# Performance work log

Hardware: AMD Instinct MI355X
Metric: run time of the kernel (lower is better)

## Reference

```python
import jax, jax.numpy as jnp
import numpy as np

N_NODES = 100000
N_EDGES = 1600000
IN_CH = 128
EMB = 64


def _init_linear(key, fan_in, fan_out):
    kw, kb = jax.random.split(key)
    scale = 1.0 / np.sqrt(fan_in)
    W = jax.random.uniform(kw, (fan_in, fan_out), jnp.float32, -scale, scale)
    b = jax.random.uniform(kb, (fan_out,), jnp.float32, -scale, scale)
    return W, b


def setup_inputs() -> dict:
    key = jax.random.key(0)
    ks = jax.random.split(key, 6)
    x = jax.random.normal(ks[0], (N_NODES, IN_CH), jnp.float32)
    edge_index = jax.random.randint(ks[1], (2, N_EDGES), 0, N_NODES)
    batch = jnp.zeros((N_NODES,), jnp.int32)
    # conv1 MLP: in_channels -> 32 -> 64 ; conv2 MLP: 64 -> 64 -> embedding_dim
    W1, b1 = _init_linear(ks[2], IN_CH, 32)
    W2, b2 = _init_linear(ks[3], 32, 64)
    W3, b3 = _init_linear(ks[4], 64, 64)
    W4, b4 = _init_linear(ks[5], 64, EMB)
    return {"x": x, "edge_index": edge_index, "batch": batch,
            "W1": W1, "b1": b1, "W2": W2, "b2": b2,
            "W3": W3, "b3": b3, "W4": W4, "b4": b4}


def _mlp(h, Wa, ba, Wb, bb):
    # PyG MLP: Linear -> act -> Linear (plain last layer)
    return jax.nn.relu(h @ Wa + ba) @ Wb + bb


def _gin_conv(x, src, dst, Wa, ba, Wb, bb):
    # out_i = MLP((1+eps)*x_i + sum_{j->i} x_j), eps = 0 (GINConv default)
    agg = jax.ops.segment_sum(x[src], dst, num_segments=N_NODES)  # [N, d]
    return _mlp(x + agg, Wa, ba, Wb, bb)


def reference(x, edge_index, batch, W1, b1, W2, b2, W3, b3, W4, b4):
    src, dst = edge_index[0], edge_index[1]
    h = jax.nn.relu(_gin_conv(x, src, dst, W1, b1, W2, b2))  # [N, 64]
    h = jax.nn.relu(_gin_conv(h, src, dst, W3, b3, W4, b4))  # [N, EMB]
    # batch is overwritten with zeros in the original forward -> single graph
    pooled = jnp.mean(h, axis=0, keepdims=True)  # [1, EMB]
    return h, pooled
```

## Files before the change

kernel.cpp:

```cpp
#include <hip/hip_runtime.h>

#define NN 100000
#define NE 1600000
#define NLB 256
#define CHUNK (NE / NLB)
#define NB 196
#define BN 512

__device__ __forceinline__ float bf2f(unsigned short u) {
    return __uint_as_float(((unsigned int)u) << 16);
}
__device__ __forceinline__ unsigned short f2bf(float f) {
    unsigned int u = __float_as_uint(f);
    return (unsigned short)((u + 0x7FFFu + ((u >> 16) & 1u)) >> 16);
}

__global__ __launch_bounds__(256) void k_front(const int* __restrict__ src,
                                               const int* __restrict__ dst,
                                               int* __restrict__ pairs,
                                               int* __restrict__ tstart,
                                               int* __restrict__ tcnt,
                                               int* __restrict__ btot,
                                               const float* __restrict__ x,
                                               const float* __restrict__ W1,
                                               unsigned short* __restrict__ z1) {
    __shared__ float Ws[128 * 32];
    __shared__ float xs[32][129];
    __shared__ int cnt[NB];
    __shared__ int sc[256];
    __shared__ int cur[NB];
    int tid = threadIdx.x;
    if (blockIdx.x < NLB) {
        int blk = blockIdx.x;
        int e0 = blk * CHUNK;
        for (int i = tid; i < NB; i += 256) cnt[i] = 0;
        __syncthreads();
        for (int i = tid; i < CHUNK; i += 256) atomicAdd(&cnt[dst[e0 + i] >> 9], 1);
        __syncthreads();
        sc[tid] = (tid < NB) ? cnt[tid] : 0;
        __syncthreads();
        for (int off = 1; off < 256; off <<= 1) {
            int v = (tid >= off) ? sc[tid - off] : 0;
            __syncthreads();
            sc[tid] += v;
            __syncthreads();
        }
        if (tid < NB) {
            int excl = sc[tid] - cnt[tid];
            cur[tid] = excl;
            tstart[blk * NB + tid] = excl;
            tcnt[blk * NB + tid]   = cnt[tid];
            atomicAdd(&btot[tid], cnt[tid]);
        }
        __syncthreads();
        for (int i = tid; i < CHUNK; i += 256) {
            int d = dst[e0 + i], s = src[e0 + i];
            int p = atomicAdd(&cur[d >> 9], 1);
            pairs[e0 + p] = ((d & (BN - 1)) << 17) | s;
        }
    } else {
        int bid = blockIdx.x - NLB;
        for (int i = tid; i < 1024; i += 256) {
            float4 w = ((const float4*)W1)[i];
            float* d = &Ws[i * 4];
            d[0] = w.x; d[1] = w.y; d[2] = w.z; d[3] = w.w;
        }
        int n_loc = tid >> 3;
        int j0    = (tid & 7) * 4;
        for (int base = bid * 32; base < NN; base += 1024 * 32) {
            __syncthreads();
            for (int t = tid; t < 1024; t += 256) {
                int n = t >> 5, c = t & 31;
                float4 v = ((const float4*)(x + (size_t)(base + n) * 128))[c];
                float* d = &xs[n][c * 4];
                d[0] = v.x; d[1] = v.y; d[2] = v.z; d[3] = v.w;
            }
            __syncthreads();
            float a0 = 0.f, a1 = 0.f, a2 = 0.f, a3 = 0.f;
            #pragma unroll 8
            for (int k = 0; k < 128; k++) {
                float xv = xs[n_loc][k];
                float4 w = *(const float4*)&Ws[k * 32 + j0];
                a0 = fmaf(xv, w.x, a0); a1 = fmaf(xv, w.y, a1);
                a2 = fmaf(xv, w.z, a2); a3 = fmaf(xv, w.w, a3);
            }
            ushort4 o = { f2bf(a0), f2bf(a1), f2bf(a2), f2bf(a3) };
            *(ushort4*)&z1[(size_t)(base + n_loc) * 32 + j0] = o;
        }
    }
}

__global__ __launch_bounds__(1024) void k_build(const int* __restrict__ pairs,
                                                const int* __restrict__ tstart,
                                                const int* __restrict__ tcnt,
                                                const int* __restrict__ btot,
                                                int* __restrict__ csr,
                                                int* __restrict__ row,
                                                int* __restrict__ rend) {
    __shared__ int segS[NLB], segL[NLB];
    __shared__ int ncnt[BN];
    __shared__ int nbase[BN + 1];
    __shared__ int sc[256];
    __shared__ int sc2[256];
    __shared__ int base_s;
    int tid = threadIdx.x, b = blockIdx.x;

    if (tid < 256) sc2[tid] = (tid < NB) ? btot[tid] : 0;
    __syncthreads();
    for (int off = 1; off < 256; off <<= 1) {
        int v = 0;
        if (tid < 256 && tid >= off) v = sc2[tid - off];
        __syncthreads();
        if (tid < 256) sc2[tid] += v;
        __syncthreads();
    }
    if (tid == 0) base_s = (b == 0) ? 0 : sc2[b - 1];
    if (tid < NLB) {
        segS[tid] = tid * CHUNK + tstart[tid * NB + b];
        segL[tid] = tcnt[tid * NB + b];
    }
    for (int i = tid; i < BN; i += 1024) ncnt[i] = 0;
    __syncthreads();

    int wave = tid >> 6, lane = tid & 63;
    for (int s = wave; s < NLB; s += 16) {
        int st = segS[s], len = segL[s];
        for (int i = lane; i < len; i += 64)
            atomicAdd(&ncnt[pairs[st + i] >> 17], 1);
    }
    __syncthreads();

    int c0 = 0, c1 = 0, tsum = 0;
    if (tid < 256) { c0 = ncnt[2 * tid]; c1 = ncnt[2 * tid + 1]; tsum = c0 + c1; sc[tid] = tsum; }
    __syncthreads();
    for (int off = 1; off < 256; off <<= 1) {
        int v = 0;
        if (tid < 256 && tid >= off) v = sc[tid - off];
        __syncthreads();
        if (tid < 256) sc[tid] += v;
        __syncthreads();
    }
    if (tid < 256) {
        int excl = sc[tid] - tsum;
        nbase[2 * tid]     = excl;
        nbase[2 * tid + 1] = excl + c0;
        if (tid == 255) nbase[BN] = sc[255];
    }
    __syncthreads();

    int base = base_s;
    if (tid < BN) {
        int n = b * BN + tid;
        if (n < NN) { row[n] = base + nbase[tid]; rend[n] = base + nbase[tid + 1]; }
        ncnt[tid] = 0;
    }
    __syncthreads();

    for (int s = wave; s < NLB; s += 16) {
        int st = segS[s], len = segL[s];
        for (int i = lane; i < len; i += 64) {
            int p = pairs[st + i];
            int ln = p >> 17;
            int pos = atomicAdd(&ncnt[ln], 1);
            csr[base + nbase[ln] + pos] = p & 0x1FFFF;
        }
    }
}

__global__ __launch_bounds__(256) void k_gather32(const int* __restrict__ row,
                                                  const int* __restrict__ rend,
                                                  const int* __restrict__ csr,
                                                  const unsigned short* __restrict__ z,
                                                  float* __restrict__ agg) {
    int n = blockIdx.x * 8 + (threadIdx.x >> 5);
    int f = threadIdx.x & 31;
    int j = row[n], e = rend[n];
    float a0 = 0.f, a1 = 0.f, a2 = 0.f, a3 = 0.f;
    for (; j + 3 < e; j += 4) {
        int i0 = csr[j], i1 = csr[j + 1], i2 = csr[j + 2], i3 = csr[j + 3];
        a0 += bf2f(z[(size_t)i0 * 32 + f]);
        a1 += bf2f(z[(size_t)i1 * 32 + f]);
        a2 += bf2f(z[(size_t)i2 * 32 + f]);
        a3 += bf2f(z[(size_t)i3 * 32 + f]);
    }
    for (; j < e; j++) a0 += bf2f(z[(size_t)csr[j] * 32 + f]);
    agg[(size_t)n * 32 + f] = (a0 + a1) + (a2 + a3);
}

__global__ __launch_bounds__(256) void k_gather64(const int* __restrict__ row,
                                                  const int* __restrict__ rend,
                                                  const int* __restrict__ csr,
                                                  const unsigned short* __restrict__ z,
                                                  float* __restrict__ agg) {
    int n = blockIdx.x * 4 + (threadIdx.x >> 6);
    int f = threadIdx.x & 63;
    int j = row[n], e = rend[n];
    float a0 = 0.f, a1 = 0.f, a2 = 0.f, a3 = 0.f;
    for (; j + 7 < e; j += 8) {
        int i0 = csr[j],     i1 = csr[j + 1], i2 = csr[j + 2], i3 = csr[j + 3];
        int i4 = csr[j + 4], i5 = csr[j + 5], i6 = csr[j + 6], i7 = csr[j + 7];
        float v0 = bf2f(z[(size_t)i0 * 64 + f]);
        float v1 = bf2f(z[(size_t)i1 * 64 + f]);
        float v2 = bf2f(z[(size_t)i2 * 64 + f]);
        float v3 = bf2f(z[(size_t)i3 * 64 + f]);
        float v4 = bf2f(z[(size_t)i4 * 64 + f]);
        float v5 = bf2f(z[(size_t)i5 * 64 + f]);
        float v6 = bf2f(z[(size_t)i6 * 64 + f]);
        float v7 = bf2f(z[(size_t)i7 * 64 + f]);
        a0 += v0 + v4; a1 += v1 + v5; a2 += v2 + v6; a3 += v3 + v7;
    }
    for (; j + 3 < e; j += 4) {
        int i0 = csr[j], i1 = csr[j + 1], i2 = csr[j + 2], i3 = csr[j + 3];
        a0 += bf2f(z[(size_t)i0 * 64 + f]);
        a1 += bf2f(z[(size_t)i1 * 64 + f]);
        a2 += bf2f(z[(size_t)i2 * 64 + f]);
        a3 += bf2f(z[(size_t)i3 * 64 + f]);
    }
    for (; j < e; j++) a0 += bf2f(z[(size_t)csr[j] * 64 + f]);
    agg[(size_t)n * 64 + f] = (a0 + a1) + (a2 + a3);
}

__global__ __launch_bounds__(256) void k_mid(const unsigned short* __restrict__ z1,
                                             const float* __restrict__ agg1,
                                             const float* __restrict__ b1,
                                             const float* __restrict__ W2,
                                             const float* __restrict__ b2,
                                             const float* __restrict__ W3,
                                             unsigned short* __restrict__ z2) {
    __shared__ float W2s[32 * 64];
    __shared__ float W3s[64 * 64];
    __shared__ float ts[32][33];
    __shared__ float hs[32 * 68];
    __shared__ float b1s[32], b2s[64];
    for (int i = threadIdx.x; i < 512; i += 256) {
        float4 w = ((const float4*)W2)[i];
        float* d = &W2s[i * 4];
        d[0] = w.x; d[1] = w.y; d[2] = w.z; d[3] = w.w;
    }
    for (int i = threadIdx.x; i < 1024; i += 256) {
        float4 w = ((const float4*)W3)[i];
        float* d = &W3s[i * 4];
        d[0] = w.x; d[1] = w.y; d[2] = w.z; d[3] = w.w;
    }
    if (threadIdx.x < 32) b1s[threadIdx.x] = b1[threadIdx.x];
    if (threadIdx.x >= 64 && threadIdx.x < 128) b2s[threadIdx.x - 64] = b2[threadIdx.x - 64];
    int n2 = threadIdx.x >> 4;
    int j0 = (threadIdx.x & 15) * 4;
    int na = 2 * n2, nb = 2 * n2 + 1;
    for (int base = blockIdx.x * 32; base < NN; base += gridDim.x * 32) {
        __syncthreads();
        #pragma unroll
        for (int r = 0; r < 4; r++) {
            int idx = threadIdx.x + 256 * r;
            int n = idx >> 5, f = idx & 31;
            ts[n][f] = fmaxf(bf2f(z1[(size_t)base * 32 + idx]) + agg1[(size_t)base * 32 + idx] + b1s[f], 0.f);
        }
        __syncthreads();
        {
            float a00=0,a01=0,a02=0,a03=0,a10=0,a11=0,a12=0,a13=0;
            #pragma unroll 8
            for (int k = 0; k < 32; k++) {
                float t0 = ts[na][k], t1 = ts[nb][k];
                float4 w = *(const float4*)&W2s[k * 64 + j0];
                a00=fmaf(t0,w.x,a00); a01=fmaf(t0,w.y,a01); a02=fmaf(t0,w.z,a02); a03=fmaf(t0,w.w,a03);
                a10=fmaf(t1,w.x,a10); a11=fmaf(t1,w.y,a11); a12=fmaf(t1,w.z,a12); a13=fmaf(t1,w.w,a13);
            }
            *(float4*)&hs[na * 68 + j0] = make_float4(fmaxf(a00+b2s[j0],0.f), fmaxf(a01+b2s[j0+1],0.f),
                                                      fmaxf(a02+b2s[j0+2],0.f), fmaxf(a03+b2s[j0+3],0.f));
            *(float4*)&hs[nb * 68 + j0] = make_float4(fmaxf(a10+b2s[j0],0.f), fmaxf(a11+b2s[j0+1],0.f),
                                                      fmaxf(a12+b2s[j0+2],0.f), fmaxf(a13+b2s[j0+3],0.f));
        }
        __syncthreads();
        {
            float a00=0,a01=0,a02=0,a03=0,a10=0,a11=0,a12=0,a13=0;
            #pragma unroll 8
            for (int k = 0; k < 64; k++) {
                float h0 = hs[na * 68 + k], h1 = hs[nb * 68 + k];
                float4 w = *(const float4*)&W3s[k * 64 + j0];
                a00=fmaf(h0,w.x,a00); a01=fmaf(h0,w.y,a01); a02=fmaf(h0,w.z,a02); a03=fmaf(h0,w.w,a03);
                a10=fmaf(h1,w.x,a10); a11=fmaf(h1,w.y,a11); a12=fmaf(h1,w.z,a12); a13=fmaf(h1,w.w,a13);
            }
            ushort4 oa = { f2bf(a00), f2bf(a01), f2bf(a02), f2bf(a03) };
            ushort4 ob = { f2bf(a10), f2bf(a11), f2bf(a12), f2bf(a13) };
            *(ushort4*)&z2[(size_t)(base + na) * 64 + j0] = oa;
            *(ushort4*)&z2[(size_t)(base + nb) * 64 + j0] = ob;
        }
    }
}

__global__ __launch_bounds__(256) void k_final(const unsigned short* __restrict__ z2,
                                               const float* __restrict__ agg2,
                                               const float* __restrict__ b3,
                                               const float* __restrict__ W4,
                                               const float* __restrict__ b4,
                                               float* __restrict__ out,
                                               float* __restrict__ gpool) {
    __shared__ float W4s[64 * 64];
    __shared__ float us[32 * 68];
    __shared__ float b3s[64], b4s[64], pool[64];
    for (int i = threadIdx.x; i < 1024; i += 256) {
        float4 w = ((const float4*)W4)[i];
        float* d = &W4s[i * 4];
        d[0] = w.x; d[1] = w.y; d[2] = w.z; d[3] = w.w;
    }
    if (threadIdx.x < 64) { b3s[threadIdx.x] = b3[threadIdx.x]; pool[threadIdx.x] = 0.f; }
    if (threadIdx.x >= 64 && threadIdx.x < 128) b4s[threadIdx.x - 64] = b4[threadIdx.x - 64];
    int n2 = threadIdx.x >> 4;
    int j0 = (threadIdx.x & 15) * 4;
    int na = 2 * n2, nb = 2 * n2 + 1;
    float p0 = 0.f, p1 = 0.f, p2 = 0.f, p3 = 0.f;
    for (int base = blockIdx.x * 32; base < NN; base += gridDim.x * 32) {
        __syncthreads();
        #pragma unroll
        for (int r = 0; r < 8; r++) {
            int idx = threadIdx.x + 256 * r;
            int n = idx >> 6, f = idx & 63;
            us[n * 68 + f] = fmaxf(bf2f(z2[(size_t)base * 64 + idx]) + agg2[(size_t)base * 64 + idx] + b3s[f], 0.f);
        }
        __syncthreads();
        float a00=0,a01=0,a02=0,a03=0,a10=0,a11=0,a12=0,a13=0;
        #pragma unroll 8
        for (int k = 0; k < 64; k++) {
            float u0 = us[na * 68 + k], u1 = us[nb * 68 + k];
            float4 w = *(const float4*)&W4s[k * 64 + j0];
            a00=fmaf(u0,w.x,a00); a01=fmaf(u0,w.y,a01); a02=fmaf(u0,w.z,a02); a03=fmaf(u0,w.w,a03);
            a10=fmaf(u1,w.x,a10); a11=fmaf(u1,w.y,a11); a12=fmaf(u1,w.z,a12); a13=fmaf(u1,w.w,a13);
        }
        float v00=fmaxf(a00+b4s[j0],0.f), v01=fmaxf(a01+b4s[j0+1],0.f);
        float v02=fmaxf(a02+b4s[j0+2],0.f), v03=fmaxf(a03+b4s[j0+3],0.f);
        float v10=fmaxf(a10+b4s[j0],0.f), v11=fmaxf(a11+b4s[j0+1],0.f);
        float v12=fmaxf(a12+b4s[j0+2],0.f), v13=fmaxf(a13+b4s[j0+3],0.f);
        *(float4*)&out[(size_t)(base + na) * 64 + j0] = make_float4(v00, v01, v02, v03);
        *(float4*)&out[(size_t)(base + nb) * 64 + j0] = make_float4(v10, v11, v12, v13);
        p0 += v00 + v10; p1 += v01 + v11; p2 += v02 + v12; p3 += v03 + v13;
    }
    __syncthreads();
    atomicAdd(&pool[j0 + 0], p0);
    atomicAdd(&pool[j0 + 1], p1);
    atomicAdd(&pool[j0 + 2], p2);
    atomicAdd(&pool[j0 + 3], p3);
    __syncthreads();
    if (threadIdx.x < 64) unsafeAtomicAdd(&gpool[threadIdx.x], pool[threadIdx.x]);
}

__global__ void k_pool(const float* __restrict__ gpool, float* __restrict__ out) {
    int t = threadIdx.x;
    if (t < 64) out[(size_t)NN * 64 + t] = gpool[t] * (1.0f / NN);
}

extern "C" void kernel_launch(void* const* d_in, const int* in_sizes, int n_in,
                              void* d_out, int out_size, void* d_ws, size_t ws_size,
                              hipStream_t stream) {
    const float* x  = (const float*)d_in[0];
    const int*   ei = (const int*)d_in[1];
    const float* W1 = (const float*)d_in[3];
    const float* b1 = (const float*)d_in[4];
    const float* W2 = (const float*)d_in[5];
    const float* b2 = (const float*)d_in[6];
    const float* W3 = (const float*)d_in[7];
    const float* b3 = (const float*)d_in[8];
    const float* W4 = (const float*)d_in[9];
    const float* b4 = (const float*)d_in[10];
    float* out = (float*)d_out;

    int*   ip     = (int*)d_ws;
    int*   tstart = ip;
    int*   tcnt   = ip + NLB * NB;
    int*   btot   = ip + 2 * NLB * NB;
    float* gpool  = (float*)(ip + 2 * NLB * NB + 196);
    int*   row    = ip + 2 * NLB * NB + 260;
    int*   rend   = row + NN;
    int*   csr    = rend + NN;
    int*   pairs  = csr + NE;
    unsigned short* z1b = (unsigned short*)(pairs + NE);
    float* agg1   = (float*)(pairs + NE + NN * 16);
    float* agg2   = (float*)pairs;
    unsigned short* z2b = (unsigned short*)(agg1 + (size_t)NN * 32);
    const int* src = ei;
    const int* dst = ei + NE;

    hipMemsetAsync(btot, 0, (196 + 64) * sizeof(int), stream);
    k_front<<<NLB + 1024, 256, 0, stream>>>(src, dst, pairs, tstart, tcnt, btot, x, W1, z1b);
    k_build<<<NB, 1024, 0, stream>>>(pairs, tstart, tcnt, btot, csr, row, rend);
    k_gather32<<<NN / 8, 256, 0, stream>>>(row, rend, csr, z1b, agg1);
    k_mid<<<1024, 256, 0, stream>>>(z1b, agg1, b1, W2, b2, W3, z2b);
    k_gather64<<<NN / 4, 256, 0, stream>>>(row, rend, csr, z2b, agg2);
    k_final<<<1024, 256, 0, stream>>>(z2b, agg2, b3, W4, b4, out, gpool);
    k_pool<<<1, 64, 0, stream>>>(gpool, out);
}
```

Before: 323.8 us.

## Vectorize CSR gathers: 8 edges per wave with wide loads and shuffle reduction

Both gather kernels now assign one 64-lane wave per node. The wave is split into 8 edge groups of 8 lanes, and each lane loads 4 or 8 packed bf16 features with a single uint2/uint4 load. Partial sums are combined across groups with xor shuffles, and the result is written with float4 stores. This replaces scalar 2-byte loads and a serial per-edge loop, aiming to raise memory-level parallelism and cut load instruction count. The cost is the shuffle reduction and idle lanes for low-degree nodes, and the 32-wide gather now launches twice as many blocks.

```diff
diff --git a/kernel.cpp b/kernel.cpp
--- a/kernel.cpp
+++ b/kernel.cpp
@@ -172,19 +172,42 @@
                                                   const int* __restrict__ csr,
                                                   const unsigned short* __restrict__ z,
                                                   float* __restrict__ agg) {
-    int n = blockIdx.x * 8 + (threadIdx.x >> 5);
-    int f = threadIdx.x & 31;
+    int n = blockIdx.x * 4 + (threadIdx.x >> 6);
+    int lane = threadIdx.x & 63;
+    int g = lane >> 3;
+    int q = lane & 7;
     int j = row[n], e = rend[n];
     float a0 = 0.f, a1 = 0.f, a2 = 0.f, a3 = 0.f;
-    for (; j + 3 < e; j += 4) {
-        int i0 = csr[j], i1 = csr[j + 1], i2 = csr[j + 2], i3 = csr[j + 3];
-        a0 += bf2f(z[(size_t)i0 * 32 + f]);
-        a1 += bf2f(z[(size_t)i1 * 32 + f]);
-        a2 += bf2f(z[(size_t)i2 * 32 + f]);
-        a3 += bf2f(z[(size_t)i3 * 32 + f]);
-    }
-    for (; j < e; j++) a0 += bf2f(z[(size_t)csr[j] * 32 + f]);
-    agg[(size_t)n * 32 + f] = (a0 + a1) + (a2 + a3);
+#define G32_BODY(J) { \
+        int idx_ = csr[(J) + g]; \
+        uint2 v_ = *(const uint2*)(z + (size_t)idx_ * 32 + q * 4); \
+        a0 += __uint_as_float(v_.x << 16); \
+        a1 += __uint_as_float(v_.x & 0xFFFF0000u); \
+        a2 += __uint_as_float(v_.y << 16); \
+        a3 += __uint_as_float(v_.y & 0xFFFF0000u); }
+    for (; j + 16 <= e; j += 16) { G32_BODY(j) G32_BODY(j + 8) }
+    if (j + 8 <= e) { G32_BODY(j) j += 8; }
+    int rem = e - j;
+    if (rem > 0) {
+        int gg = (g < rem) ? g : (rem - 1);
+        int idx_ = csr[j + gg];
+        uint2 v_ = *(const uint2*)(z + (size_t)idx_ * 32 + q * 4);
+        if (g < rem) {
+            a0 += __uint_as_float(v_.x << 16);
+            a1 += __uint_as_float(v_.x & 0xFFFF0000u);
+            a2 += __uint_as_float(v_.y << 16);
+            a3 += __uint_as_float(v_.y & 0xFFFF0000u);
+        }
+    }
+#undef G32_BODY
+    #pragma unroll
+    for (int m = 8; m < 64; m <<= 1) {
+        a0 += __shfl_xor(a0, m);
+        a1 += __shfl_xor(a1, m);
+        a2 += __shfl_xor(a2, m);
+        a3 += __shfl_xor(a3, m);
+    }
+    if (g == 0) *(float4*)&agg[(size_t)n * 32 + q * 4] = make_float4(a0, a1, a2, a3);
 }
 
 __global__ __launch_bounds__(256) void k_gather64(const int* __restrict__ row,
@@ -193,31 +216,45 @@
                                                   const unsigned short* __restrict__ z,
                                                   float* __restrict__ agg) {
     int n = blockIdx.x * 4 + (threadIdx.x >> 6);
-    int f = threadIdx.x & 63;
+    int lane = threadIdx.x & 63;
+    int g = lane >> 3;
+    int q = lane & 7;
     int j = row[n], e = rend[n];
     float a0 = 0.f, a1 = 0.f, a2 = 0.f, a3 = 0.f;
-    for (; j + 7 < e; j += 8) {
-        int i0 = csr[j],     i1 = csr[j + 1], i2 = csr[j + 2], i3 = csr[j + 3];
-        int i4 = csr[j + 4], i5 = csr[j + 5], i6 = csr[j + 6], i7 = csr[j + 7];
-        float v0 = bf2f(z[(size_t)i0 * 64 + f]);
-        float v1 = bf2f(z[(size_t)i1 * 64 + f]);
-        float v2 = bf2f(z[(size_t)i2 * 64 + f]);
-        float v3 = bf2f(z[(size_t)i3 * 64 + f]);
-        float v4 = bf2f(z[(size_t)i4 * 64 + f]);
-        float v5 = bf2f(z[(size_t)i5 * 64 + f]);
-        float v6 = bf2f(z[(size_t)i6 * 64 + f]);
-        float v7 = bf2f(z[(size_t)i7 * 64 + f]);
-        a0 += v0 + v4; a1 += v1 + v5; a2 += v2 + v6; a3 += v3 + v7;
-    }
-    for (; j + 3 < e; j += 4) {
-        int i0 = csr[j], i1 = csr[j + 1], i2 = csr[j + 2], i3 = csr[j + 3];
-        a0 += bf2f(z[(size_t)i0 * 64 + f]);
-        a1 += bf2f(z[(size_t)i1 * 64 + f]);
-        a2 += bf2f(z[(size_t)i2 * 64 + f]);
-        a3 += bf2f(z[(size_t)i3 * 64 + f]);
-    }
-    for (; j < e; j++) a0 += bf2f(z[(size_t)csr[j] * 64 + f]);
-    agg[(size_t)n * 64 + f] = (a0 + a1) + (a2 + a3);
+    float a4 = 0.f, a5 = 0.f, a6 = 0.f, a7 = 0.f;
+#define G64_BODY(J) { \
+        int idx_ = csr[(J) + g]; \
+        uint4 v_ = *(const uint4*)(z + (size_t)idx_ * 64 + q * 8); \
+        a0 += __uint_as_float(v_.x << 16); a1 += __uint_as_float(v_.x & 0xFFFF0000u); \
+        a2 += __uint_as_float(v_.y << 16); a3 += __uint_as_float(v_.y & 0xFFFF0000u); \
+        a4 += __uint_as_float(v_.z << 16); a5 += __uint_as_float(v_.z & 0xFFFF0000u); \
+        a6 += __uint_as_float(v_.w << 16); a7 += __uint_as_float(v_.w & 0xFFFF0000u); }
+    for (; j + 16 <= e; j += 16) { G64_BODY(j) G64_BODY(j + 8) }
+    if (j + 8 <= e) { G64_BODY(j) j += 8; }
+    int rem = e - j;
+    if (rem > 0) {
+        int gg = (g < rem) ? g : (rem - 1);
+        int idx_ = csr[j + gg];
+        uint4 v_ = *(const uint4*)(z + (size_t)idx_ * 64 + q * 8);
+        if (g < rem) {
+            a0 += __uint_as_float(v_.x << 16); a1 += __uint_as_float(v_.x & 0xFFFF0000u);
+            a2 += __uint_as_float(v_.y << 16); a3 += __uint_as_float(v_.y & 0xFFFF0000u);
+            a4 += __uint_as_float(v_.z << 16); a5 += __uint_as_float(v_.z & 0xFFFF0000u);
+            a6 += __uint_as_float(v_.w << 16); a7 += __uint_as_float(v_.w & 0xFFFF0000u);
+        }
+    }
+#undef G64_BODY
+    #pragma unroll
+    for (int m = 8; m < 64; m <<= 1) {
+        a0 += __shfl_xor(a0, m); a1 += __shfl_xor(a1, m);
+        a2 += __shfl_xor(a2, m); a3 += __shfl_xor(a3, m);
+        a4 += __shfl_xor(a4, m); a5 += __shfl_xor(a5, m);
+        a6 += __shfl_xor(a6, m); a7 += __shfl_xor(a7, m);
+    }
+    if (g == 0) {
+        *(float4*)&agg[(size_t)n * 64 + q * 8]     = make_float4(a0, a1, a2, a3);
+        *(float4*)&agg[(size_t)n * 64 + q * 8 + 4] = make_float4(a4, a5, a6, a7);
+    }
 }
 
 __global__ __launch_bounds__(256) void k_mid(const unsigned short* __restrict__ z1,
@@ -382,7 +419,7 @@
     hipMemsetAsync(btot, 0, (196 + 64) * sizeof(int), stream);
     k_front<<<NLB + 1024, 256, 0, stream>>>(src, dst, pairs, tstart, tcnt, btot, x, W1, z1b);
     k_build<<<NB, 1024, 0, stream>>>(pairs, tstart, tcnt, btot, csr, row, rend);
-    k_gather32<<<NN / 8, 256, 0, stream>>>(row, rend, csr, z1b, agg1);
+    k_gather32<<<NN / 4, 256, 0, stream>>>(row, rend, csr, z1b, agg1);
     k_mid<<<1024, 256, 0, stream>>>(z1b, agg1, b1, W2, b2, W3, z2b);
     k_gather64<<<NN / 4, 256, 0, stream>>>(row, rend, csr, z2b, agg2);
     k_final<<<1024, 256, 0, stream>>>(z2b, agg2, b3, W4, b4, out, gpool);
```

Measured after the change: 312.1 us. -3.6%, faster.
